# Kernel tuning notes

Measured on AMD Instinct MI355X. Metric: run time of the kernel, lower is better.

Reference implementation:

```python
import jax, jax.numpy as jnp
import numpy as np
import math

EMBED = 1024
HEADS = 16
HEAD_DIM = EMBED // HEADS


def setup_inputs() -> dict:
    key = jax.random.key(0)
    ks = jax.random.split(key, 9)
    B, S = 2, 2048
    query = jax.random.normal(ks[0], (B, S, EMBED), dtype=jnp.float32)
    key_t = jax.random.normal(ks[1], (B, S, EMBED), dtype=jnp.float32)
    value = jax.random.normal(ks[2], (B, S, EMBED), dtype=jnp.float32)
    mask = jax.random.randint(ks[3], (B, 1, S, S), 0, 2, dtype=jnp.int32)
    # nn.Linear(head_dim, head_dim, bias=False) weights: [out, in]
    sc = 1.0 / math.sqrt(HEAD_DIM)
    Wq = jax.random.uniform(ks[4], (HEAD_DIM, HEAD_DIM), jnp.float32, -sc, sc)
    Wk = jax.random.uniform(ks[5], (HEAD_DIM, HEAD_DIM), jnp.float32, -sc, sc)
    Wv = jax.random.uniform(ks[6], (HEAD_DIM, HEAD_DIM), jnp.float32, -sc, sc)
    so = 1.0 / math.sqrt(EMBED)
    Wo = jax.random.uniform(ks[7], (EMBED, EMBED), jnp.float32, -so, so)
    bo = jax.random.uniform(ks[8], (EMBED,), jnp.float32, -so, so)
    return {"query": query, "key": key_t, "value": value, "mask": mask,
            "Wq": Wq, "Wk": Wk, "Wv": Wv, "Wo": Wo, "bo": bo}


def reference(query, key, value, mask, Wq, Wk, Wv, Wo, bo):
    B, Sq, E = query.shape
    Sk = key.shape[1]
    H, D = HEADS, HEAD_DIM
    # Faithful raw reshape into heads (as in the torch source, no transpose)
    q = query.reshape(B, H, Sq, D)
    k = key.reshape(B, H, Sk, D)
    v = value.reshape(B, H, Sk, D)
    # per-head_dim Linear (bias-free): x @ W.T
    Q = jnp.einsum('bhsd,ed->bhse', q, Wq)
    K = jnp.einsum('bhsd,ed->bhse', k, Wk)
    V = jnp.einsum('bhsd,ed->bhse', v, Wv)
    scores = jnp.einsum('bhqd,bhkd->bhqk', Q, K)  # [B,H,Sq,Sk]
    scores = jnp.where(mask == 0, jnp.float32(-1e20), scores)
    # NOTE: source divides by sqrt(embed_size), not sqrt(head_dim)
    attn = jax.nn.softmax(scores / jnp.float32(math.sqrt(E)), axis=-1)
    out = jnp.einsum('bhqk,bhkd->bhqd', attn, V).reshape(B, Sq, H * D)
    return out @ Wo.T + bo
```

## Files before the change

kernel.cpp:

```cpp
#include <hip/hip_runtime.h>

typedef __attribute__((ext_vector_type(8))) short short8;
typedef __attribute__((ext_vector_type(4))) float f32x4;
typedef __attribute__((ext_vector_type(2))) int int2v;
typedef __attribute__((ext_vector_type(4))) int int4v;

__device__ __forceinline__ short f2bf(float f) {
  unsigned u = __builtin_bit_cast(unsigned, f);
  u += 0x7fff + ((u >> 16) & 1);
  return (short)(u >> 16);
}

__device__ __forceinline__ int pk2bf(float lo, float hi) {
#if defined(__gfx950__) && __has_builtin(__builtin_amdgcn_cvt_pk_bf16_f32)
  typedef __attribute__((ext_vector_type(2))) __bf16 bf16x2;
  bf16x2 v = __builtin_amdgcn_cvt_pk_bf16_f32(lo, hi);
  return __builtin_bit_cast(int, v);
#else
  return (int)(unsigned short)(short)f2bf(lo) | (((int)f2bf(hi)) << 16);
#endif
}

__device__ __forceinline__ int pktr(float lo, float hi) {
  return (int)(__builtin_bit_cast(unsigned, lo) >> 16) |
         (int)(__builtin_bit_cast(unsigned, hi) & 0xffff0000u);
}

__device__ __forceinline__ short8 pack8(f32x4 a, f32x4 b) {
  int4v t;
  t.x = pk2bf(a[0], a[1]);
  t.y = pk2bf(a[2], a[3]);
  t.z = pk2bf(b[0], b[1]);
  t.w = pk2bf(b[2], b[3]);
  return __builtin_bit_cast(short8, t);
}

__device__ __forceinline__ float fand(float p, int m) {
  return __builtin_bit_cast(float, __builtin_bit_cast(int, p) & m);
}

__device__ __forceinline__ int bmask(unsigned w, int bit) {
#if __has_builtin(__builtin_amdgcn_sbfe)
  return __builtin_amdgcn_sbfe((int)w, bit, 1);
#else
  return ((int)(w << (31 - bit))) >> 31;
#endif
}

__device__ __forceinline__ float fexp2(float x) {
#if __has_builtin(__builtin_amdgcn_exp2f)
  return __builtin_amdgcn_exp2f(x);
#else
  return exp2f(x);
#endif
}

__device__ __forceinline__ void glds16(const short* g, short* lbase, int lane) {
#if __has_builtin(__builtin_amdgcn_global_load_lds)
  __builtin_amdgcn_global_load_lds(
      (const __attribute__((address_space(1))) unsigned int*)g,
      (__attribute__((address_space(3))) unsigned int*)lbase, 16, 0, 0);
#else
  *(short8*)(lbase + lane * 8) = *(const short8*)g;
#endif
}

__global__ __launch_bounds__(256) void prep(const float* __restrict__ q,
                                            const float* __restrict__ k,
                                            const float* __restrict__ v,
                                            const float* __restrict__ Wq,
                                            const float* __restrict__ Wk,
                                            const float* __restrict__ Wv,
                                            const float* __restrict__ Wo,
                                            const int* __restrict__ mask,
                                            short* __restrict__ Qp,
                                            short* __restrict__ Kp,
                                            short* __restrict__ Vtp,
                                            short* __restrict__ Wob,
                                            unsigned* __restrict__ mmod) {
  const int bid = blockIdx.x;
  const int tid = threadIdx.x;

  if (bid >= 4096) {
    const int mb = bid - 4096;
    const int kp = mb & 15, bq = mb >> 4;
    const int b_ = bq >> 5, q64 = bq & 31;
    const int wv = tid >> 6, qd = (tid >> 4) & 3, m16_ = tid & 15;
    unsigned d = 0;
#pragma unroll
    for (int hb = 0; hb < 2; ++hb) {
      const int ka = kp * 2 + hb;
#pragma unroll
      for (int r = 0; r < 4; ++r) {
        const int* mr = mask + b_ * 4194304 +
                        (q64 * 64 + wv * 16 + qd * 4 + r) * 2048 + ka * 64 + m16_;
#pragma unroll
        for (int nt = 0; nt < 4; ++nt)
          if (mr[nt * 16] != 0) d |= 1u << (hb * 16 + r * 4 + nt);
      }
    }
    mmod[mb * 256 + tid] = d;
    return;
  }
  if (bid >= 3072) {
    const int i = ((bid - 3072) * 256 + tid) * 4;
    const f32x4 x = *(const f32x4*)&Wo[i];
    int2v o;
    o.x = pk2bf(x[0], x[1]);
    o.y = pk2bf(x[2], x[3]);
    *(int2v*)&Wob[i] = o;
    return;
  }

  __shared__ short xt[64][72];
  __shared__ short ot[64][72];
  const int mode = bid >> 10;
  const int bt = bid & 1023;
  const float* X;
  const float* W;
  float scale;
  if (mode == 0) { X = q; W = Wq; scale = 0.045084220f; }
  else if (mode == 1) { X = k; W = Wk; scale = 1.0f; }
  else { X = v; W = Wv; scale = 1.0f; }

  const int r0 = bt * 64;
  const int row = tid >> 2, seg = (tid & 3) * 16;
  const f32x4* xs = (const f32x4*)(X + (r0 + row) * 64 + seg);
  const f32x4 x0 = xs[0], x1 = xs[1], x2 = xs[2], x3 = xs[3];
  *(short8*)&xt[row][seg] = pack8(x0, x1);
  *(short8*)&xt[row][seg + 8] = pack8(x2, x3);
  __syncthreads();

  const int lane = tid & 63, wave = tid >> 6;
  const int m16 = lane & 15, quad = lane >> 4;

  const short8 a0 = *(const short8*)&xt[wave * 16 + m16][quad * 8];
  const short8 a1 = *(const short8*)&xt[wave * 16 + m16][32 + quad * 8];

  f32x4 acc[4];
#pragma unroll
  for (int nt = 0; nt < 4; ++nt) {
    const f32x4* wp0 = (const f32x4*)&W[(nt * 16 + m16) * 64 + quad * 8];
    const f32x4* wp1 = (const f32x4*)&W[(nt * 16 + m16) * 64 + 32 + quad * 8];
    const short8 b0 = pack8(wp0[0], wp0[1]);
    const short8 b1 = pack8(wp1[0], wp1[1]);
    f32x4 z = (f32x4){0.f, 0.f, 0.f, 0.f};
    z = __builtin_amdgcn_mfma_f32_16x16x32_bf16(a0, b0, z, 0, 0, 0);
    z = __builtin_amdgcn_mfma_f32_16x16x32_bf16(a1, b1, z, 0, 0, 0);
    acc[nt] = z;
  }

  if (mode != 2) {
#pragma unroll
    for (int nt = 0; nt < 4; ++nt)
#pragma unroll
      for (int r = 0; r < 4; ++r)
        ot[wave * 16 + quad * 4 + r][nt * 16 + m16] = f2bf(acc[nt][r] * scale);
  } else {
#pragma unroll
    for (int nt = 0; nt < 4; ++nt)
#pragma unroll
      for (int r = 0; r < 4; ++r)
        ot[nt * 16 + m16][16 * quad + 4 * r + wave] = f2bf(acc[nt][r]);
  }
  __syncthreads();

  const int orow = tid >> 2, opart = tid & 3;
  if (mode != 2) {
    short* dst = (mode == 0 ? Qp : Kp) + (r0 + orow) * 64 + opart * 16;
    *(short8*)&dst[0] = *(const short8*)&ot[orow][opart * 16];
    *(short8*)&dst[8] = *(const short8*)&ot[orow][opart * 16 + 8];
  } else {
    const int bh = r0 >> 11, s0 = r0 & 2047;
    short* dst = Vtp + bh * 131072 + orow * 2048 + s0 + opart * 16;
    *(short8*)&dst[0] = *(const short8*)&ot[orow][opart * 16];
    *(short8*)&dst[8] = *(const short8*)&ot[orow][opart * 16 + 8];
  }
}

__global__ __launch_bounds__(256) void flash64f(const short* __restrict__ Qp,
                                                const short* __restrict__ Kp,
                                                const short* __restrict__ Vt,
                                                const unsigned* __restrict__ mmod,
                                                short* __restrict__ Ob) {
  __shared__ __attribute__((aligned(16))) short kt[4096];
  __shared__ __attribute__((aligned(16))) short vt[4096];
  __shared__ __attribute__((aligned(16))) short pt[64][72];
  const int tid = threadIdx.x;
  const int bid = blockIdx.x;
  const int local = bid >> 3;
  const int qblk = local & 31;
  const int bh = (bid & 7) * 4 + (local >> 5);
  const int q0 = qblk << 6;
  const int b = bh >> 4;
  const short* Qh = Qp + bh * 131072;
  const short* Kh = Kp + bh * 131072;
  const short* Vh = Vt + bh * 131072;
  const int lane = tid & 63, wave = tid >> 6;
  const int m16 = lane & 15, quad = lane >> 4;
  const int srow = lane >> 3, sj = (lane & 7) ^ srow;
  const int msh = m16 * 4;
  const int koff = m16 * 128 + ((quad ^ (m16 & 7)) * 16);
  const unsigned* mq = mmod + ((b * 32 + qblk) * 16) * 256 + tid;

  short8 aq[2];
#pragma unroll
  for (int h = 0; h < 2; ++h)
    aq[h] = *(const short8*)&Qh[(q0 + wave * 16 + m16) * 64 + h * 32 + quad * 8];

  float l[4] = {0.f, 0.f, 0.f, 0.f};
  f32x4 oacc[4];
#pragma unroll
  for (int dt = 0; dt < 4; ++dt) oacc[dt] = (f32x4){0.f, 0.f, 0.f, 0.f};

  for (int kk = 0; kk < 16; ++kk) {
    const unsigned mw = mq[kk * 256];
#pragma unroll
    for (int h = 0; h < 2; ++h) {
      const int ka = kk * 2 + h;
      const int k0 = ka << 6;
      __syncthreads();
#pragma unroll
      for (int t = 0; t < 2; ++t) {
        const int crow = wave * 16 + t * 8;
        glds16(Kh + (ka * 64 + crow + srow) * 64 + sj * 8, kt + crow * 64, lane);
        glds16(Vh + (crow + srow) * 2048 + k0 + sj * 8, vt + crow * 64, lane);
      }
      __syncthreads();

      f32x4 s[4];
#pragma unroll
      for (int nt = 0; nt < 4; ++nt) {
        const int o0 = nt * 2048 + koff;
        const short8 kb0 = *(const short8*)((const char*)kt + o0);
        const short8 kb1 = *(const short8*)((const char*)kt + (o0 ^ 64));
        f32x4 z = (f32x4){0.f, 0.f, 0.f, 0.f};
        z = __builtin_amdgcn_mfma_f32_16x16x32_bf16(aq[0], kb0, z, 0, 0, 0);
        z = __builtin_amdgcn_mfma_f32_16x16x32_bf16(aq[1], kb1, z, 0, 0, 0);
        s[nt] = z;
      }

      const int bitbase = h * 16;
#pragma unroll
      for (int r = 0; r < 4; ++r) {
        float p[4];
#pragma unroll
        for (int nt = 0; nt < 4; ++nt)
          p[nt] = fand(fexp2(s[nt][r]), bmask(mw, bitbase + r * 4 + nt));
        l[r] += (p[0] + p[1]) + (p[2] + p[3]);
        int2v pp;
        pp.x = pktr(p[0], p[1]);
        pp.y = pktr(p[2], p[3]);
        *(int2v*)&pt[wave * 16 + quad * 4 + r][msh] = pp;
      }

      const short8 ap0 = *(const short8*)&pt[wave * 16 + m16][quad * 8];
      const short8 ap1 = *(const short8*)&pt[wave * 16 + m16][32 + quad * 8];
#pragma unroll
      for (int dt = 0; dt < 4; ++dt) {
        const int o0 = dt * 2048 + koff;
        const short8 vb0 = *(const short8*)((const char*)vt + o0);
        const short8 vb1 = *(const short8*)((const char*)vt + (o0 ^ 64));
        f32x4 z = oacc[dt];
        z = __builtin_amdgcn_mfma_f32_16x16x32_bf16(ap0, vb0, z, 0, 0, 0);
        z = __builtin_amdgcn_mfma_f32_16x16x32_bf16(ap1, vb1, z, 0, 0, 0);
        oacc[dt] = z;
      }
    }
  }

#pragma unroll
  for (int r = 0; r < 4; ++r) {
#pragma unroll
    for (int off = 1; off < 16; off <<= 1) l[r] += __shfl_xor(l[r], off, 16);
    const float inv = 1.0f / l[r];
#pragma unroll
    for (int dt = 0; dt < 4; ++dt)
      pt[wave * 16 + quad * 4 + r][dt * 16 + m16] = f2bf(oacc[dt][r] * inv);
  }

  const int orow = lane >> 2, opart = lane & 3;
  const int prow = wave * 16 + orow;
  short* og = Ob + (bh * 2048 + q0 + prow) * 64 + opart * 16;
  *(short8*)&og[0] = *(const short8*)&pt[prow][opart * 16];
  *(short8*)&og[8] = *(const short8*)&pt[prow][opart * 16 + 8];
}

__global__ __launch_bounds__(256) void outproj(const short* __restrict__ Ob,
                                               const short* __restrict__ Wob,
                                               const float* __restrict__ bo,
                                               float* __restrict__ out) {
  __shared__ short at[64][72];
  __shared__ short bt[128][72];
  const int tid = threadIdx.x;
  const int bid = blockIdx.x;
  const int ct = bid >> 6, rt = bid & 63;
  const int r0 = rt * 64, c0 = ct * 128;
  const int lane = tid & 63, wave = tid >> 6;
  const int mr = (wave >> 1) * 32, nc = (wave & 1) * 64;
  const int m16 = lane & 15, quad = lane >> 4;
  const int arow = tid >> 2, apart = tid & 3;
  const int brow = tid >> 1, bhalf = (tid & 1) * 32;

  f32x4 acc[2][4];
#pragma unroll
  for (int mt = 0; mt < 2; ++mt)
#pragma unroll
    for (int nt = 0; nt < 4; ++nt) acc[mt][nt] = (f32x4){0.f, 0.f, 0.f, 0.f};

  for (int kc = 0; kc < 16; ++kc) {
    __syncthreads();
    const short* ag = &Ob[(r0 + arow) * 1024 + kc * 64 + apart * 16];
    const short* bg = &Wob[(c0 + brow) * 1024 + kc * 64 + bhalf];
    *(short8*)&at[arow][apart * 16] = *(const short8*)&ag[0];
    *(short8*)&at[arow][apart * 16 + 8] = *(const short8*)&ag[8];
    *(short8*)&bt[brow][bhalf] = *(const short8*)&bg[0];
    *(short8*)&bt[brow][bhalf + 8] = *(const short8*)&bg[8];
    *(short8*)&bt[brow][bhalf + 16] = *(const short8*)&bg[16];
    *(short8*)&bt[brow][bhalf + 24] = *(const short8*)&bg[24];
    __syncthreads();

#pragma unroll
    for (int kh = 0; kh < 2; ++kh) {
      short8 af[2], bf[4];
#pragma unroll
      for (int i = 0; i < 2; ++i)
        af[i] = *(const short8*)&at[mr + i * 16 + m16][kh * 32 + quad * 8];
#pragma unroll
      for (int j = 0; j < 4; ++j)
        bf[j] = *(const short8*)&bt[nc + j * 16 + m16][kh * 32 + quad * 8];
#pragma unroll
      for (int mt = 0; mt < 2; ++mt)
#pragma unroll
        for (int nt = 0; nt < 4; ++nt)
          acc[mt][nt] = __builtin_amdgcn_mfma_f32_16x16x32_bf16(af[mt], bf[nt], acc[mt][nt], 0, 0, 0);
    }
  }

#pragma unroll
  for (int nt = 0; nt < 4; ++nt) {
    const int col = c0 + nc + nt * 16 + m16;
    const float bias = bo[col];
#pragma unroll
    for (int mt = 0; mt < 2; ++mt)
#pragma unroll
      for (int rr2 = 0; rr2 < 4; ++rr2)
        out[(r0 + mr + mt * 16 + quad * 4 + rr2) * 1024 + col] = acc[mt][nt][rr2] + bias;
  }
}

extern "C" void kernel_launch(void* const* d_in, const int* in_sizes, int n_in,
                              void* d_out, int out_size, void* d_ws, size_t ws_size,
                              hipStream_t stream) {
  const float* query = (const float*)d_in[0];
  const float* key = (const float*)d_in[1];
  const float* value = (const float*)d_in[2];
  const int* mask = (const int*)d_in[3];
  const float* Wq = (const float*)d_in[4];
  const float* Wk = (const float*)d_in[5];
  const float* Wv = (const float*)d_in[6];
  const float* Wo = (const float*)d_in[7];
  const float* bo = (const float*)d_in[8];
  float* out = (float*)d_out;

  char* ws = (char*)d_ws;
  short* Qp = (short*)(ws);
  short* Kp = (short*)(ws + 8388608);
  short* Vt = (short*)(ws + 16777216);
  short* Ob = (short*)(ws + 25165824);
  short* Wob = (short*)(ws + 41943040);
  unsigned* mmod = (unsigned*)(ws + 44564480);

  prep<<<5120, 256, 0, stream>>>(query, key, value, Wq, Wk, Wv, Wo, mask,
                                 Qp, Kp, Vt, Wob, mmod);
  flash64f<<<1024, 256, 0, stream>>>(Qp, Kp, Vt, mmod, Ob);
  outproj<<<512, 256, 0, stream>>>(Ob, Wob, bo, out);
}
```

Before: 239.1 us.

## Double-buffer K/V tiles in flash kernel and swizzle P scratch layout

The flash attention kernel now keeps two LDS buffers for K and V tiles, so the global-to-LDS load of the next tile is issued before computing on the current one. Each tile step then needs a single barrier instead of two __syncthreads. The P tile in LDS changes from a padded [64][72] array to an XOR-swizzled 64x64 layout to avoid bank conflicts, and s_setprio raises wave priority around the MFMA blocks. LDS use grows, which may lower occupancy.

```diff
diff --git a/kernel.cpp b/kernel.cpp
--- a/kernel.cpp
+++ b/kernel.cpp
@@ -183,9 +183,11 @@
                                                 const short* __restrict__ Vt,
                                                 const unsigned* __restrict__ mmod,
                                                 short* __restrict__ Ob) {
-  __shared__ __attribute__((aligned(16))) short kt[4096];
-  __shared__ __attribute__((aligned(16))) short vt[4096];
-  __shared__ __attribute__((aligned(16))) short pt[64][72];
+  __shared__ __attribute__((aligned(16))) short kt0[4096];
+  __shared__ __attribute__((aligned(16))) short kt1[4096];
+  __shared__ __attribute__((aligned(16))) short vt0[4096];
+  __shared__ __attribute__((aligned(16))) short vt1[4096];
+  __shared__ __attribute__((aligned(16))) short pt[4096];
   const int tid = threadIdx.x;
   const int bid = blockIdx.x;
   const int local = bid >> 3;
@@ -199,10 +201,19 @@
   const int lane = tid & 63, wave = tid >> 6;
   const int m16 = lane & 15, quad = lane >> 4;
   const int srow = lane >> 3, sj = (lane & 7) ^ srow;
-  const int msh = m16 * 4;
   const int koff = m16 * 128 + ((quad ^ (m16 & 7)) * 16);
   const unsigned* mq = mmod + ((b * 32 + qblk) * 16) * 256 + tid;
 
+  char* const ptB = (char*)pt;
+  int woff[4];
+#pragma unroll
+  for (int r = 0; r < 4; ++r)
+    woff[r] = (wave * 16 + quad * 4 + r) * 128 +
+              ((m16 * 8) ^ (((quad * 4 + r) & 7) << 4));
+  const int aswz = (m16 & 7) << 4;
+  const int aoff0 = (wave * 16 + m16) * 128 + ((quad * 16) ^ aswz);
+  const int aoff1 = (wave * 16 + m16) * 128 + ((quad * 16 + 64) ^ aswz);
+
   short8 aq[2];
 #pragma unroll
   for (int h = 0; h < 2; ++h)
@@ -213,59 +224,82 @@
 #pragma unroll
   for (int dt = 0; dt < 4; ++dt) oacc[dt] = (f32x4){0.f, 0.f, 0.f, 0.f};
 
+  auto stage = [&](short* ktb, short* vtb, int ka) {
+#pragma unroll
+    for (int t = 0; t < 2; ++t) {
+      const int crow = wave * 16 + t * 8;
+      glds16(Kh + (ka * 64 + crow + srow) * 64 + sj * 8, ktb + crow * 64, lane);
+      glds16(Vh + (crow + srow) * 2048 + ka * 64 + sj * 8, vtb + crow * 64, lane);
+    }
+  };
+
+  auto compute = [&](const short* ktp, const short* vtp, unsigned mw, int bitbase) {
+    const char* ktb = (const char*)ktp;
+    const char* vtb = (const char*)vtp;
+    f32x4 s[4];
+    __builtin_amdgcn_s_setprio(1);
+#pragma unroll
+    for (int nt = 0; nt < 4; ++nt) {
+      const int o0 = nt * 2048 + koff;
+      const short8 kb0 = *(const short8*)(ktb + o0);
+      const short8 kb1 = *(const short8*)(ktb + (o0 ^ 64));
+      f32x4 z = (f32x4){0.f, 0.f, 0.f, 0.f};
+      z = __builtin_amdgcn_mfma_f32_16x16x32_bf16(aq[0], kb0, z, 0, 0, 0);
+      z = __builtin_amdgcn_mfma_f32_16x16x32_bf16(aq[1], kb1, z, 0, 0, 0);
+      s[nt] = z;
+    }
+    __builtin_amdgcn_s_setprio(0);
+
+#pragma unroll
+    for (int r = 0; r < 4; ++r) {
+      float p[4];
+#pragma unroll
+      for (int nt = 0; nt < 4; ++nt)
+        p[nt] = fand(fexp2(s[nt][r]), bmask(mw, bitbase + r * 4 + nt));
+      l[r] += (p[0] + p[1]) + (p[2] + p[3]);
+      int2v pp;
+      pp.x = pktr(p[0], p[1]);
+      pp.y = pktr(p[2], p[3]);
+      *(int2v*)(ptB + woff[r]) = pp;
+    }
+
+    const short8 ap0 = *(const short8*)(ptB + aoff0);
+    const short8 ap1 = *(const short8*)(ptB + aoff1);
+    __builtin_amdgcn_s_setprio(1);
+#pragma unroll
+    for (int dt = 0; dt < 4; ++dt) {
+      const int o0 = dt * 2048 + koff;
+      const short8 vb0 = *(const short8*)(vtb + o0);
+      const short8 vb1 = *(const short8*)(vtb + (o0 ^ 64));
+      f32x4 z = oacc[dt];
+      z = __builtin_amdgcn_mfma_f32_16x16x32_bf16(ap0, vb0, z, 0, 0, 0);
+      z = __builtin_amdgcn_mfma_f32_16x16x32_bf16(ap1, vb1, z, 0, 0, 0);
+      oacc[dt] = z;
+    }
+    __builtin_amdgcn_s_setprio(0);
+  };
+
+  unsigned mw = mq[0];
+  stage(kt0, vt0, 0);
+  asm volatile("s_waitcnt vmcnt(0)" ::: "memory");
+  __builtin_amdgcn_s_barrier();
+
   for (int kk = 0; kk < 16; ++kk) {
-    const unsigned mw = mq[kk * 256];
-#pragma unroll
-    for (int h = 0; h < 2; ++h) {
-      const int ka = kk * 2 + h;
-      const int k0 = ka << 6;
-      __syncthreads();
-#pragma unroll
-      for (int t = 0; t < 2; ++t) {
-        const int crow = wave * 16 + t * 8;
-        glds16(Kh + (ka * 64 + crow + srow) * 64 + sj * 8, kt + crow * 64, lane);
-        glds16(Vh + (crow + srow) * 2048 + k0 + sj * 8, vt + crow * 64, lane);
-      }
-      __syncthreads();
-
-      f32x4 s[4];
-#pragma unroll
-      for (int nt = 0; nt < 4; ++nt) {
-        const int o0 = nt * 2048 + koff;
-        const short8 kb0 = *(const short8*)((const char*)kt + o0);
-        const short8 kb1 = *(const short8*)((const char*)kt + (o0 ^ 64));
-        f32x4 z = (f32x4){0.f, 0.f, 0.f, 0.f};
-        z = __builtin_amdgcn_mfma_f32_16x16x32_bf16(aq[0], kb0, z, 0, 0, 0);
-        z = __builtin_amdgcn_mfma_f32_16x16x32_bf16(aq[1], kb1, z, 0, 0, 0);
-        s[nt] = z;
-      }
-
-      const int bitbase = h * 16;
-#pragma unroll
-      for (int r = 0; r < 4; ++r) {
-        float p[4];
-#pragma unroll
-        for (int nt = 0; nt < 4; ++nt)
-          p[nt] = fand(fexp2(s[nt][r]), bmask(mw, bitbase + r * 4 + nt));
-        l[r] += (p[0] + p[1]) + (p[2] + p[3]);
-        int2v pp;
-        pp.x = pktr(p[0], p[1]);
-        pp.y = pktr(p[2], p[3]);
-        *(int2v*)&pt[wave * 16 + quad * 4 + r][msh] = pp;
-      }
-
-      const short8 ap0 = *(const short8*)&pt[wave * 16 + m16][quad * 8];
-      const short8 ap1 = *(const short8*)&pt[wave * 16 + m16][32 + quad * 8];
-#pragma unroll
-      for (int dt = 0; dt < 4; ++dt) {
-        const int o0 = dt * 2048 + koff;
-        const short8 vb0 = *(const short8*)((const char*)vt + o0);
-        const short8 vb1 = *(const short8*)((const char*)vt + (o0 ^ 64));
-        f32x4 z = oacc[dt];
-        z = __builtin_amdgcn_mfma_f32_16x16x32_bf16(ap0, vb0, z, 0, 0, 0);
-        z = __builtin_amdgcn_mfma_f32_16x16x32_bf16(ap1, vb1, z, 0, 0, 0);
-        oacc[dt] = z;
-      }
+    stage(kt1, vt1, 2 * kk + 1);
+    compute(kt0, vt0, mw, 0);
+    asm volatile("s_waitcnt vmcnt(0)" ::: "memory");
+    __builtin_amdgcn_s_barrier();
+
+    unsigned mwn = 0u;
+    if (kk < 15) {
+      mwn = mq[(kk + 1) * 256];
+      stage(kt0, vt0, 2 * kk + 2);
+    }
+    compute(kt1, vt1, mw, 16);
+    mw = mwn;
+    if (kk < 15) {
+      asm volatile("s_waitcnt vmcnt(0)" ::: "memory");
+      __builtin_amdgcn_s_barrier();
     }
   }
 
@@ -276,14 +310,17 @@
     const float inv = 1.0f / l[r];
 #pragma unroll
     for (int dt = 0; dt < 4; ++dt)
-      pt[wave * 16 + quad * 4 + r][dt * 16 + m16] = f2bf(oacc[dt][r] * inv);
+      *(short*)(ptB + (wave * 16 + quad * 4 + r) * 128 +
+                ((dt * 32 + m16 * 2) ^ (((quad * 4 + r) & 7) << 4))) =
+          f2bf(oacc[dt][r] * inv);
   }
 
   const int orow = lane >> 2, opart = lane & 3;
   const int prow = wave * 16 + orow;
+  const int oswz = (orow & 7) << 4;
   short* og = Ob + (bh * 2048 + q0 + prow) * 64 + opart * 16;
-  *(short8*)&og[0] = *(const short8*)&pt[prow][opart * 16];
-  *(short8*)&og[8] = *(const short8*)&pt[prow][opart * 16 + 8];
+  *(short8*)&og[0] = *(const short8*)(ptB + prow * 128 + ((opart * 32) ^ oswz));
+  *(short8*)&og[8] = *(const short8*)(ptB + prow * 128 + ((opart * 32 + 16) ^ oswz));
 }
 
 __global__ __launch_bounds__(256) void outproj(const short* __restrict__ Ob,
```

Result: faster. 229.8 us (-3.9%).
